# Kernel optimization log

Hardware: AMD Instinct MI355X
Metric: run time of the kernel (lower is better)

## Reference

```python
import jax, jax.numpy as jnp
import numpy as np


def setup_inputs() -> dict:
    key = jax.random.key(0)
    k0, k1, k2, k3 = jax.random.split(key, 4)
    B, C, L1, L2, U = 256, 128, 32, 32, 128
    return {
        "inputs": jax.random.normal(k0, (B, C, L1, L2), jnp.float32),
        "W": jax.random.normal(k1, (C + 3 * U, 7 * U), jnp.float32) * 0.05,
        "Umat": jax.random.normal(k2, (3 * U, U), jnp.float32) * 0.05,
        "bias": jnp.zeros((8 * U,), jnp.float32),
        "w_ij": jax.random.normal(k3, (C, U), jnp.float32) * 0.05,
    }


def _hard_sigmoid(x):
    # keras hard_sigmoid
    return jnp.clip(0.2 * x + 0.5, 0.0, 1.0)


def _spatial_gru(inputs, W, Umat, bias, w_ij):
    B, C, L1, L2 = inputs.shape
    U = w_ij.shape[1]
    wr, wz = W[:, : 3 * U], W[:, 3 * U : 7 * U]
    br, bz, b_ij = bias[: 3 * U], bias[3 * U : 7 * U], bias[7 * U :]
    s = jnp.transpose(inputs, (2, 3, 0, 1))  # (L1, L2, B, C)
    h0 = jnp.zeros((B, U), inputs.dtype)

    def cell(h_left, inp):
        h_diag, h_top, s_ij = inp  # each (B, U) / (B, C)
        # q = [h_top, h_left, h_diag, s_ij]  (B, 3U + C)
        q = jnp.concatenate([h_top, h_left, h_diag, s_ij], axis=1)
        r = _hard_sigmoid(q @ wr + br)                      # (B, 3U)
        z = q @ wz + bz                                     # (B, 4U)
        # softmax across the 4 gates per unit (softmax_by_row)
        zg = jax.nn.softmax(z.reshape(B, 4, U), axis=1)
        zi, zl, zt, zd = zg[:, 0], zg[:, 1], zg[:, 2], zg[:, 3]
        hij_ = jnp.tanh(
            s_ij @ w_ij + b_ij
            + (r * jnp.concatenate([h_left, h_top, h_diag], axis=1)) @ Umat
        )
        hij = zl * h_left + zt * h_top + zd * h_diag + zi * hij_
        return hij, hij

    def row(prev_row, s_row):
        # prev_row: (L2+1, B, U) hidden states of row above, boundary h0 at col 0
        # h_diag_j = prev_row[j], h_top_j = prev_row[j+1]
        _, row_h = jax.lax.scan(cell, h0, (prev_row[:-1], prev_row[1:], s_row))
        new_row = jnp.concatenate([h0[None], row_h], axis=0)  # (L2+1, B, U)
        return new_row, None

    init_row = jnp.zeros((L2 + 1, B, U), inputs.dtype)
    last_row, _ = jax.lax.scan(row, init_row, s)
    return last_row[-1]  # h at bottom-right cell, (B, U)


def reference(inputs, W, Umat, bias, w_ij):
    return _spatial_gru(inputs, W, Umat, bias, w_ij)
```

## Files before the change

### kernel.cpp

```cpp
#include <hip/hip_runtime.h>
#include <hip/hip_bf16.h>

typedef _Float16 f16x8 __attribute__((ext_vector_type(8)));
typedef float f32x4 __attribute__((ext_vector_type(4)));

#define BATCH 256
#define UD 128
#define K1 512
#define LDA 520
#define LDA2 392
#define CELLSZ (BATCH*UD)
#define RINGSZ (32*CELLSZ)

__global__ void k_reorder(const float* __restrict__ in, _Float16* __restrict__ X){
  int b = blockIdx.x, i = blockIdx.y;
  __shared__ float tile[128][33];
  int tid = threadIdx.x;
#pragma unroll
  for (int r=0;r<16;++r){
    int c = r*8 + (tid>>5), j = tid&31;
    tile[c][j] = in[(((size_t)b*128 + c)*32 + i)*32 + j];
  }
  __syncthreads();
#pragma unroll
  for (int r=0;r<16;++r){
    int j = r*2 + (tid>>7), c = tid&127;
    X[((size_t)(i*32 + j)*256 + b)*128 + c] = (_Float16)tile[c][j];
  }
}

__global__ void k_prep(const float* __restrict__ W,
                       const float* __restrict__ Um,
                       const float* __restrict__ wij,
                       _Float16* __restrict__ WT, _Float16* __restrict__ B2T,
                       unsigned* __restrict__ cnt){
  int idx = blockIdx.x*256 + threadIdx.x;
  if (idx < 256) cnt[idx] = 0u;
  if (idx < 896*512){
    int n = idx >> 9, k = idx & 511;
    WT[idx] = (_Float16)W[k*896 + n];
  }
  if (idx < 128*512){
    int n = idx >> 9, k = idx & 511;
    float v = (k < 384) ? Um[k*128 + n] : wij[(k-384)*128 + n];
    B2T[idx] = (_Float16)v;
  }
}

__device__ __forceinline__ void strip_bar(unsigned* __restrict__ c, unsigned target){
  __syncthreads();
  if (threadIdx.x == 0){
    __hip_atomic_fetch_add(c, 1u, __ATOMIC_RELEASE, __HIP_MEMORY_SCOPE_AGENT);
    while (__hip_atomic_load(c, __ATOMIC_RELAXED, __HIP_MEMORY_SCOPE_AGENT) < target)
      __builtin_amdgcn_s_sleep(8);
    (void)__hip_atomic_load(c, __ATOMIC_ACQUIRE, __HIP_MEMORY_SCOPE_AGENT);
  }
  __syncthreads();
}

__global__ __launch_bounds__(256, 2) void k_sweep(
    const _Float16* __restrict__ X,
    float* __restrict__ ring,
    const _Float16* __restrict__ WT,
    const _Float16* __restrict__ B2T,
    const float* __restrict__ bias,
    float* __restrict__ out,
    unsigned* __restrict__ cnt)
{
  __shared__ __align__(16) _Float16 Al[32*LDA];
  __shared__ __align__(16) _Float16 A2l[32*LDA2];

  const int tid  = threadIdx.x;
  const int wave = tid >> 6;
  const int lane = tid & 63;
  const int l15  = lane & 15;
  const int quad = lane >> 4;

  const int cellslot = blockIdx.x >> 3;
  const int strip    = blockIdx.x & 7;
  const int bs = strip * 32;
  unsigned* mycnt = cnt + strip*32;

  for (int d = 0; d < 63; ++d){
    const int i0  = (d > 31) ? (d - 31) : 0;
    const int ihi = (d < 31) ? d : 31;
    const int nc  = ihi - i0 + 1;

    if (cellslot < nc){
      const int i = i0 + cellslot;
      const int j = d - i;

      const bool hasT = (i >= 1);
      const bool hasL = (j >= 1);
      const bool hasD = hasT && hasL;

      const float* rm1 = ring + (size_t)((d+2)%3)*RINGSZ;
      const float* rm2 = ring + (size_t)((d+1)%3)*RINGSZ;
      float*       rw  = ring + (size_t)(d%3)*RINGSZ;

      const float* hTop  = rm1 + (size_t)(i-1)*CELLSZ;
      const float* hLeft = rm1 + (size_t)i*CELLSZ;
      const float* hDiag = rm2 + (size_t)(i-1)*CELLSZ;
      float*       hOut  = rw  + (size_t)i*CELLSZ;
      const _Float16* Xc = X + (size_t)(i*32 + j)*CELLSZ;

      {
        const float* srcs[3];
        srcs[0] = hasT ? hTop : nullptr;
        srcs[1] = hasL ? hLeft : nullptr;
        srcs[2] = hasD ? hDiag : nullptr;
#pragma unroll
        for (int r=0;r<3;++r){
          const float* src = srcs[r];
          if (src){
            for (int v = tid; v < 1024; v += 256){
              int m = v >> 5, kc = (v & 31) << 2;
              float4 f = *(const float4*)(src + (size_t)(bs+m)*UD + kc);
              union { _Float16 h[4]; ushort4 u; } p;
              p.h[0]=(_Float16)f.x; p.h[1]=(_Float16)f.y;
              p.h[2]=(_Float16)f.z; p.h[3]=(_Float16)f.w;
              *(ushort4*)&Al[m*LDA + r*128 + kc] = p.u;
            }
          } else {
            for (int v = tid; v < 1024; v += 256){
              int m = v >> 5, kc = (v & 31) << 2;
              *(ushort4*)&Al[m*LDA + r*128 + kc] = make_ushort4(0,0,0,0);
            }
          }
        }
        for (int v = tid; v < 512; v += 256){
          int m = v >> 4, kc = (v & 15) << 3;
          *(uint4*)&Al[m*LDA + 384 + kc] = *(const uint4*)(Xc + (size_t)(bs+m)*UD + kc);
        }
      }
      __syncthreads();

      f32x4 acc[2][14];
#pragma unroll
      for (int a=0;a<2;++a)
#pragma unroll
        for (int t=0;t<14;++t) acc[a][t] = (f32x4){0.f,0.f,0.f,0.f};

      {
        const _Float16* bptr[14];
#pragma unroll
        for (int t=0;t<14;++t){
          const int n = (t<6) ? (wave*96 + t*16)
                              : (384 + ((t-6)>>1)*128 + wave*32 + ((t-6)&1)*16);
          bptr[t] = WT + (size_t)(n + l15)*K1 + quad*8;
        }
#pragma unroll
        for (int ks=0; ks<16; ++ks){
          const int kb = ks*32 + quad*8;
          f16x8 a0 = *(const f16x8*)&Al[l15*LDA + kb];
          f16x8 a1 = *(const f16x8*)&Al[(16+l15)*LDA + kb];
          f16x8 b[14];
#pragma unroll
          for (int t=0;t<14;++t) b[t] = *(const f16x8*)(bptr[t] + ks*32);
#pragma unroll
          for (int t=0;t<14;++t){
            acc[0][t] = __builtin_amdgcn_mfma_f32_16x16x32_f16(a0, b[t], acc[0][t], 0,0,0);
            acc[1][t] = __builtin_amdgcn_mfma_f32_16x16x32_f16(a1, b[t], acc[1][t], 0,0,0);
          }
        }
      }

#pragma unroll
      for (int mt=0;mt<2;++mt)
#pragma unroll
        for (int t=0;t<6;++t){
          const int col = wave*96 + t*16 + l15;
          const float br = bias[col];
          const int hcol = (col < 128) ? (128 + col) : ((col < 256) ? (col - 128) : col);
#pragma unroll
          for (int rg=0;rg<4;++rg){
            const int m = mt*16 + quad*4 + rg;
            float r = 0.2f*(acc[mt][t][rg] + br) + 0.5f;
            r = fminf(fmaxf(r, 0.f), 1.f);
            float h = (float)Al[m*LDA + hcol];
            A2l[m*LDA2 + col] = (_Float16)(r*h);
          }
        }
      __syncthreads();

      f32x4 acc2[2][2];
#pragma unroll
      for (int a=0;a<2;++a){ acc2[a][0]=(f32x4){0.f,0.f,0.f,0.f}; acc2[a][1]=(f32x4){0.f,0.f,0.f,0.f}; }
      {
        const _Float16* b2ptr[2];
#pragma unroll
        for (int s=0;s<2;++s) b2ptr[s] = B2T + (size_t)(wave*32 + s*16 + l15)*K1 + quad*8;
#pragma unroll
        for (int ks=0; ks<16; ++ks){
          const int kb = ks*32 + quad*8;
          f16x8 a0, a1;
          if (ks < 12){
            a0 = *(const f16x8*)&A2l[l15*LDA2 + kb];
            a1 = *(const f16x8*)&A2l[(16+l15)*LDA2 + kb];
          } else {
            a0 = *(const f16x8*)&Al[l15*LDA + kb];
            a1 = *(const f16x8*)&Al[(16+l15)*LDA + kb];
          }
#pragma unroll
          for (int s=0;s<2;++s){
            f16x8 b = *(const f16x8*)(b2ptr[s] + ks*32);
            acc2[0][s] = __builtin_amdgcn_mfma_f32_16x16x32_f16(a0, b, acc2[0][s], 0,0,0);
            acc2[1][s] = __builtin_amdgcn_mfma_f32_16x16x32_f16(a1, b, acc2[1][s], 0,0,0);
          }
        }
      }

#pragma unroll
      for (int mt=0;mt<2;++mt)
#pragma unroll
        for (int s=0;s<2;++s){
          const int u = wave*32 + s*16 + l15;
          const float bz0 = bias[384 + 0*128 + u];
          const float bz1 = bias[384 + 1*128 + u];
          const float bz2 = bias[384 + 2*128 + u];
          const float bz3 = bias[384 + 3*128 + u];
          const float bij = bias[896 + u];
#pragma unroll
          for (int rg=0;rg<4;++rg){
            const int m = mt*16 + quad*4 + rg;
            const size_t row = (size_t)(bs+m)*UD + u;
            float z0 = acc[mt][6 + 0 + s][rg] + bz0;
            float z1 = acc[mt][6 + 2 + s][rg] + bz1;
            float z2 = acc[mt][6 + 4 + s][rg] + bz2;
            float z3 = acc[mt][6 + 6 + s][rg] + bz3;
            float mx = fmaxf(fmaxf(z0,z1), fmaxf(z2,z3));
            float e0 = __expf(z0-mx), e1 = __expf(z1-mx), e2 = __expf(z2-mx), e3 = __expf(z3-mx);
            float inv = 1.f/(e0+e1+e2+e3);
            float hl = hasL ? hLeft[row] : 0.f;
            float ht = hasT ? hTop[row]  : 0.f;
            float hd = hasD ? hDiag[row] : 0.f;
            float cand = tanhf(acc2[mt][s][rg] + bij);
            float hv = (e1*hl + e2*ht + e3*hd + e0*cand)*inv;
            hOut[row] = hv;
            if (d == 62) out[row] = hv;
          }
        }
    }

    if (d < 62) strip_bar(mycnt, (unsigned)(d+1)*32u);
  }
}

extern "C" void kernel_launch(void* const* d_in, const int* in_sizes, int n_in,
                              void* d_out, int out_size, void* d_ws, size_t ws_size,
                              hipStream_t stream){
  const float* inp  = (const float*)d_in[0];
  const float* W    = (const float*)d_in[1];
  const float* Um   = (const float*)d_in[2];
  const float* bias = (const float*)d_in[3];
  const float* wij  = (const float*)d_in[4];
  float* out = (float*)d_out;

  char* ws = (char*)d_ws;
  _Float16* WT   = (_Float16*)(ws);
  _Float16* B2T  = (_Float16*)(ws + 917504);
  _Float16* X    = (_Float16*)(ws + 1048576);
  float*    ring = (float*)   (ws + 68157440);
  unsigned* cnt  = (unsigned*)(ws + 80740352);

  k_reorder<<<dim3(256,32),256,0,stream>>>(inp, X);
  k_prep<<<1792,256,0,stream>>>(W, Um, wij, WT, B2T, cnt);
  k_sweep<<<256,256,0,stream>>>(X, ring, WT, B2T, bias, out, cnt);
}
```

Baseline: 3.105 ms.

## Relax barrier ordering and use atomic ring loads/stores with LDS-sourced hidden states

The inter-block strip barrier drops its release/acquire semantics in favour of relaxed atomics plus a compiler fence, and shortens the sleep interval. To stay coherent without those fences, ring buffer reads and writes become relaxed agent-scope atomic 8-byte loads and 4-byte stores, which should bypass the non-coherent cache path. The gating epilogue now reads h_left, h_top and h_diag from the fp16 copies already staged in LDS instead of re-reading fp32 values from global memory, trading some precision for less traffic. The goal is lower barrier and fence cost per wavefront step, at the risk of memory-ordering correctness and narrower atomic loads.

```diff
diff --git a/kernel.cpp b/kernel.cpp
--- a/kernel.cpp
+++ b/kernel.cpp
@@ -50,12 +50,18 @@
 __device__ __forceinline__ void strip_bar(unsigned* __restrict__ c, unsigned target){
   __syncthreads();
   if (threadIdx.x == 0){
-    __hip_atomic_fetch_add(c, 1u, __ATOMIC_RELEASE, __HIP_MEMORY_SCOPE_AGENT);
+    __hip_atomic_fetch_add(c, 1u, __ATOMIC_RELAXED, __HIP_MEMORY_SCOPE_AGENT);
     while (__hip_atomic_load(c, __ATOMIC_RELAXED, __HIP_MEMORY_SCOPE_AGENT) < target)
-      __builtin_amdgcn_s_sleep(8);
-    (void)__hip_atomic_load(c, __ATOMIC_ACQUIRE, __HIP_MEMORY_SCOPE_AGENT);
+      __builtin_amdgcn_s_sleep(4);
+    asm volatile("" ::: "memory");
   }
   __syncthreads();
+}
+
+__device__ __forceinline__ float2 ld_ring8(const float* p){
+  unsigned long long q = __hip_atomic_load((const unsigned long long*)p,
+      __ATOMIC_RELAXED, __HIP_MEMORY_SCOPE_AGENT);
+  union { unsigned long long u; float2 f; } v; v.u = q; return v.f;
 }
 
 __global__ __launch_bounds__(256, 2) void k_sweep(
@@ -113,13 +119,20 @@
         for (int r=0;r<3;++r){
           const float* src = srcs[r];
           if (src){
-            for (int v = tid; v < 1024; v += 256){
-              int m = v >> 5, kc = (v & 31) << 2;
-              float4 f = *(const float4*)(src + (size_t)(bs+m)*UD + kc);
-              union { _Float16 h[4]; ushort4 u; } p;
-              p.h[0]=(_Float16)f.x; p.h[1]=(_Float16)f.y;
-              p.h[2]=(_Float16)f.z; p.h[3]=(_Float16)f.w;
-              *(ushort4*)&Al[m*LDA + r*128 + kc] = p.u;
+            float2 f[8];
+#pragma unroll
+            for (int it=0;it<8;++it){
+              int v = tid + it*256;
+              int m = v >> 6, p = (v & 63) << 1;
+              f[it] = ld_ring8(src + (size_t)(bs+m)*UD + p);
+            }
+#pragma unroll
+            for (int it=0;it<8;++it){
+              int v = tid + it*256;
+              int m = v >> 6, p = (v & 63) << 1;
+              union { _Float16 h[2]; unsigned u; } pk;
+              pk.h[0] = (_Float16)f[it].x; pk.h[1] = (_Float16)f[it].y;
+              *(unsigned*)&Al[m*LDA + r*128 + p] = pk.u;
             }
           } else {
             for (int v = tid; v < 1024; v += 256){
@@ -231,12 +244,12 @@
             float mx = fmaxf(fmaxf(z0,z1), fmaxf(z2,z3));
             float e0 = __expf(z0-mx), e1 = __expf(z1-mx), e2 = __expf(z2-mx), e3 = __expf(z3-mx);
             float inv = 1.f/(e0+e1+e2+e3);
-            float hl = hasL ? hLeft[row] : 0.f;
-            float ht = hasT ? hTop[row]  : 0.f;
-            float hd = hasD ? hDiag[row] : 0.f;
+            float ht = (float)Al[m*LDA +   0 + u];
+            float hl = (float)Al[m*LDA + 128 + u];
+            float hd = (float)Al[m*LDA + 256 + u];
             float cand = tanhf(acc2[mt][s][rg] + bij);
             float hv = (e1*hl + e2*ht + e3*hd + e0*cand)*inv;
-            hOut[row] = hv;
+            __hip_atomic_store(&hOut[row], hv, __ATOMIC_RELAXED, __HIP_MEMORY_SCOPE_AGENT);
             if (d == 62) out[row] = hv;
           }
         }
```

Measured after the change: 3.030 ms. 2.4% less time.
